# Performance work log

Measured on AMD Instinct MI355X. Metric: run time of the kernel, lower is better.

Reference implementation:

```python
import jax, jax.numpy as jnp
import numpy as np

H = 4
N_PAPER, N_AUTHOR = 100000, 50000
F_IN = 128
HID, OUT = 128, 64  # total channels (per-head = total // H)


def setup_inputs() -> dict:
    key = jax.random.key(0)
    ks = jax.random.split(key, 20)
    inp = {
        'x_paper': jax.random.normal(ks[0], (N_PAPER, F_IN), jnp.float32),
        'x_author': jax.random.normal(ks[1], (N_AUTHOR, F_IN), jnp.float32),
        'src_pp': jax.random.randint(ks[2], (1600000,), 0, N_PAPER, jnp.int32),
        'dst_pp': jax.random.randint(ks[3], (1600000,), 0, N_PAPER, jnp.int32),
        'src_ap': jax.random.randint(ks[4], (800000,), 0, N_AUTHOR, jnp.int32),
        'dst_ap': jax.random.randint(ks[5], (800000,), 0, N_PAPER, jnp.int32),
        'src_pa': jax.random.randint(ks[6], (800000,), 0, N_PAPER, jnp.int32),
        'dst_pa': jax.random.randint(ks[7], (800000,), 0, N_AUTHOR, jnp.int32),
    }
    # Per-edge-type (3 relations) GATConv params, stacked on axis 0.
    s1 = 1.0 / np.sqrt(F_IN)
    s2 = 1.0 / np.sqrt(HID)
    inp['Wsrc1'] = jax.random.normal(ks[8], (3, F_IN, HID), jnp.float32) * s1
    inp['Wdst1'] = jax.random.normal(ks[9], (3, F_IN, HID), jnp.float32) * s1
    inp['asrc1'] = jax.random.normal(ks[10], (3, H, HID // H), jnp.float32) * s1
    inp['adst1'] = jax.random.normal(ks[11], (3, H, HID // H), jnp.float32) * s1
    inp['b1'] = jnp.zeros((3, HID), jnp.float32)
    inp['Wsrc2'] = jax.random.normal(ks[12], (3, HID, OUT), jnp.float32) * s2
    inp['Wdst2'] = jax.random.normal(ks[13], (3, HID, OUT), jnp.float32) * s2
    inp['asrc2'] = jax.random.normal(ks[14], (3, H, OUT // H), jnp.float32) * s2
    inp['adst2'] = jax.random.normal(ks[15], (3, H, OUT // H), jnp.float32) * s2
    inp['b2'] = jnp.zeros((3, OUT), jnp.float32)
    return inp


def gat_conv(xs, xd, src, dst, Ws, Wd, a_s, a_d, b, n_dst):
    """Bipartite GATConv (PyG semantics, add_self_loops=False, concat=True)."""
    C = a_s.shape[-1]
    hs = (xs @ Ws).reshape(xs.shape[0], H, C)   # [Ns,H,C]
    hd = (xd @ Wd).reshape(xd.shape[0], H, C)   # [Nd,H,C]
    es = jnp.sum(hs * a_s, axis=-1)             # [Ns,H]
    ed = jnp.sum(hd * a_d, axis=-1)             # [Nd,H]
    e = jax.nn.leaky_relu(es[src] + ed[dst], negative_slope=0.2)  # [E,H]
    m = jax.ops.segment_max(e, dst, num_segments=n_dst)
    m = jnp.where(jnp.isfinite(m), m, 0.0)
    ee = jnp.exp(e - m[dst])
    denom = jax.ops.segment_sum(ee, dst, num_segments=n_dst)
    alpha = ee / (denom[dst] + 1e-16)           # softmax over incoming edges
    out = jax.ops.segment_sum(alpha[:, :, None] * hs[src], dst, num_segments=n_dst)
    return out.reshape(n_dst, H * C) + b


def reference(x_paper, x_author, src_pp, dst_pp, src_ap, dst_ap, src_pa, dst_pa,
              Wsrc1, Wdst1, asrc1, adst1, b1, Wsrc2, Wdst2, asrc2, adst2, b2):
    def layer(xp, xa, Ws, Wd, a_s, a_d, b):
        # to_hetero: one conv per relation, sum-aggregate per dst node type
        op = gat_conv(xp, xp, src_pp, dst_pp, Ws[0], Wd[0], a_s[0], a_d[0], b[0], N_PAPER)
        op = op + gat_conv(xa, xp, src_ap, dst_ap, Ws[1], Wd[1], a_s[1], a_d[1], b[1], N_PAPER)
        oa = gat_conv(xp, xa, src_pa, dst_pa, Ws[2], Wd[2], a_s[2], a_d[2], b[2], N_AUTHOR)
        return op, oa

    hp, ha = layer(x_paper, x_author, Wsrc1, Wdst1, asrc1, adst1, b1)
    hp, ha = jax.nn.relu(hp), jax.nn.relu(ha)
    op, oa = layer(hp, ha, Wsrc2, Wdst2, asrc2, adst2, b2)
    # concat node types along axis 0: [N_PAPER + N_AUTHOR, OUT]
    return jnp.concatenate([op, oa], axis=0)
```

## Files before the change

### kernel.cpp

```cpp
#include <hip/hip_runtime.h>


#define LEAKY(x) ((x) > 0.f ? (x) : 0.2f * (x))
#define ECH 4096
#define NBMAX 784

typedef _Float16 h8 __attribute__((ext_vector_type(8)));
typedef _Float16 h2 __attribute__((ext_vector_type(2)));
typedef float f4 __attribute__((ext_vector_type(4)));

__launch_bounds__(256)
__global__ void bucket_scatter_chunked(
    const int* __restrict__ s0, const int* __restrict__ d0, int E0,
    int* __restrict__ bc0, int* __restrict__ bt0, int C0, int NB0, int c0,
    const int* __restrict__ s1, const int* __restrict__ d1, int E1,
    int* __restrict__ bc1, int* __restrict__ bt1, int C1, int NB1, int c1,
    const int* __restrict__ s2, const int* __restrict__ d2, int E2,
    int* __restrict__ bc2, int* __restrict__ bt2, int C2, int NB2) {
    __shared__ int lcnt[NBMAX], lbase[NBMAX];
    int ch = blockIdx.x;
    const int* src; const int* dst; int* bc; int* bt; int cap, NB, E;
    if (ch < c0)            { src = s0; dst = d0; bc = bc0; bt = bt0; cap = C0; NB = NB0; E = E0; }
    else if (ch < c0 + c1)  { ch -= c0; src = s1; dst = d1; bc = bc1; bt = bt1; cap = C1; NB = NB1; E = E1; }
    else                    { ch -= c0 + c1; src = s2; dst = d2; bc = bc2; bt = bt2; cap = C2; NB = NB2; E = E2; }
    int t = threadIdx.x;
    int ebeg = ch * ECH;
    int eend = ebeg + ECH < E ? ebeg + ECH : E;

    for (int b = t; b < NB; b += 256) lcnt[b] = 0;
    __syncthreads();
    for (int i = ebeg + t; i < eend; i += 256) atomicAdd(&lcnt[dst[i] >> 7], 1);
    __syncthreads();
    for (int b = t; b < NB; b += 256) {
        int c = lcnt[b];
        lbase[b] = c ? atomicAdd(&bc[b], c) : 0;
        lcnt[b] = 0;
    }
    __syncthreads();
    for (int i = ebeg + t; i < eend; i += 256) {
        int d = dst[i], b = d >> 7;
        int p = lbase[b] + atomicAdd(&lcnt[b], 1);
        if (p < cap) bt[(size_t)b * cap + p] = src[i] | ((d & 127) << 20);
    }
}

__launch_bounds__(256)
__global__ void bucket_build(
    const int* __restrict__ bt0, const int* __restrict__ bc0, int* __restrict__ ss0,
    int* __restrict__ beg0, int* __restrict__ end0, int NB0, int C0, int Nd0,
    const int* __restrict__ bt1, const int* __restrict__ bc1, int* __restrict__ ss1,
    int* __restrict__ beg1, int* __restrict__ end1, int NB1, int C1, int Nd1,
    const int* __restrict__ bt2, const int* __restrict__ bc2, int* __restrict__ ss2,
    int* __restrict__ beg2, int* __restrict__ end2, int NB2, int C2, int Nd2) {
    __shared__ int hist[128], pre[129], cur[128];
    int bb = blockIdx.x;
    const int* bt; const int* bcp; int* ssp; int* bg; int* en; int cap, nd;
    if (bb < NB0)            { bt = bt0; bcp = bc0; ssp = ss0; bg = beg0; en = end0; cap = C0; nd = Nd0; }
    else if (bb < NB0 + NB1) { bb -= NB0; bt = bt1; bcp = bc1; ssp = ss1; bg = beg1; en = end1; cap = C1; nd = Nd1; }
    else                     { bb -= NB0 + NB1; bt = bt2; bcp = bc2; ssp = ss2; bg = beg2; en = end2; cap = C2; nd = Nd2; }
    int tid = threadIdx.x;
    int n = bcp[bb]; if (n > cap) n = cap;
    const int* btb = bt + (size_t)bb * cap;
    int ssbase = bb * cap;
    int dbase = bb << 7;

    if (tid < 128) hist[tid] = 0;
    __syncthreads();
    for (int i = tid; i < n; i += 256) atomicAdd(&hist[btb[i] >> 20], 1);
    __syncthreads();
    if (tid < 128) pre[tid + 1] = hist[tid];
    if (tid == 0) pre[0] = 0;
    __syncthreads();
    for (int off = 1; off < 128; off <<= 1) {
        int v = 0;
        if (tid < 128) {
            int i = tid + 1;
            v = pre[i] + ((i > off) ? pre[i - off] : 0);
        }
        __syncthreads();
        if (tid < 128) pre[tid + 1] = v;
        __syncthreads();
    }
    if (tid < 128) {
        int d = dbase + tid;
        if (d < nd) {
            int b_ = ssbase + pre[tid];
            bg[d] = b_;
            en[d] = b_ + hist[tid];
        }
        cur[tid] = 0;
    }
    __syncthreads();
    for (int i = tid; i < n; i += 256) {
        int v = btb[i];
        int dl = v >> 20;
        int p = atomicAdd(&cur[dl], 1);
        ssp[ssbase + pre[dl] + p] = v & 0xFFFFF;
    }
}

__launch_bounds__(512)
__global__ void prep(const float* __restrict__ Wdst1, const float* __restrict__ adst1,
                     const float* __restrict__ Wdst2, const float* __restrict__ adst2,
                     const float* __restrict__ Wsrc1, const float* __restrict__ Wsrc2,
                     const float* __restrict__ b1, const float* __restrict__ b2,
                     float* __restrict__ WDA, _Float16* __restrict__ Wt,
                     float* __restrict__ bsum) {
    int r = blockIdx.x, t = threadIdx.x;
    if (r < 6) {
        int f = t >> 2, h = t & 3;
        const float* Wd; const float* ad; int Ncol, C;
        if (r < 3) { Wd = Wdst1 + r * 16384; ad = adst1 + r * 128; Ncol = 128; C = 32; }
        else       { Wd = Wdst2 + (r - 3) * 8192; ad = adst2 + (r - 3) * 64; Ncol = 64; C = 16; }
        float s = 0.f;
        for (int c = 0; c < C; ++c) s += Wd[f * Ncol + h * C + c] * ad[h * C + c];
        WDA[r * 512 + f * 4 + h] = s;
    } else if (r < 12) {
        int rr = r - 6;
        const float* W; _Float16* o; int BN;
        if (rr < 3) { W = Wsrc1 + rr * 16384; o = Wt + rr * 16384; BN = 128; }
        else        { W = Wsrc2 + (rr - 3) * 8192; o = Wt + 3 * 16384 + (rr - 3) * 8192; BN = 64; }
        for (int idx = t; idx < BN * 128; idx += 512) {
            int n = idx >> 7, k = idx & 127;
            o[idx] = (_Float16)W[k * BN + n];
        }
    } else {
        if (t < 128) bsum[t] = b1[t] + b1[128 + t];
        else if (t < 192) bsum[128 + (t - 128)] = b2[t - 128] + b2[64 + (t - 128)];
    }
}

__launch_bounds__(256)
__global__ void conv_ed(const float* __restrict__ xp, const float* __restrict__ xa,
                        int NP, int NA, _Float16* __restrict__ xph, _Float16* __restrict__ xah,
                        const float* __restrict__ WDA,
                        float* __restrict__ EDpp, float* __restrict__ EDap,
                        float* __restrict__ EDpa) {
    int wid = blockIdx.x * 4 + (threadIdx.x >> 6);
    if (wid >= NP + NA) return;
    int lane = threadIdx.x & 63;
    const float* x; _Float16* xh; const float4* W0; const float4* W1;
    float* e0p; float* e1p; int row;
    if (wid < NP) { row = wid; x = xp; xh = xph; W0 = (const float4*)WDA;
                    W1 = (const float4*)(WDA + 512); e0p = EDpp; e1p = EDap; }
    else { row = wid - NP; x = xa; xh = xah; W0 = (const float4*)(WDA + 1024);
           W1 = nullptr; e0p = EDpa; e1p = nullptr; }
    float2 xv = *(const float2*)(x + (size_t)row * 128 + lane * 2);
    h2 hv = {(_Float16)xv.x, (_Float16)xv.y};
    *(h2*)(xh + (size_t)row * 128 + lane * 2) = hv;
    float4 a0 = W0[lane * 2], a1 = W0[lane * 2 + 1];
    float4 p = make_float4(xv.x * a0.x + xv.y * a1.x, xv.x * a0.y + xv.y * a1.y,
                           xv.x * a0.z + xv.y * a1.z, xv.x * a0.w + xv.y * a1.w);
    float4 q = make_float4(0.f, 0.f, 0.f, 0.f);
    if (W1) {
        float4 b0 = W1[lane * 2], b1 = W1[lane * 2 + 1];
        q = make_float4(xv.x * b0.x + xv.y * b1.x, xv.x * b0.y + xv.y * b1.y,
                        xv.x * b0.z + xv.y * b1.z, xv.x * b0.w + xv.y * b1.w);
    }
#pragma unroll
    for (int off = 32; off; off >>= 1) {
        p.x += __shfl_xor(p.x, off); p.y += __shfl_xor(p.y, off);
        p.z += __shfl_xor(p.z, off); p.w += __shfl_xor(p.w, off);
        q.x += __shfl_xor(q.x, off); q.y += __shfl_xor(q.y, off);
        q.z += __shfl_xor(q.z, off); q.w += __shfl_xor(q.w, off);
    }
    if (lane == 0) {
        *(float4*)(e0p + (size_t)row * 4) = p;
        if (e1p) *(float4*)(e1p + (size_t)row * 4) = q;
    }
}

template <int BN>
__launch_bounds__(256)
__global__ void gemm3(const _Float16* __restrict__ A0, int M0, const _Float16* __restrict__ W0,
                      const float* __restrict__ as0, _Float16* __restrict__ O0, float* __restrict__ es0,
                      const _Float16* __restrict__ A1, int M1, const _Float16* __restrict__ W1,
                      const float* __restrict__ as1, _Float16* __restrict__ O1, float* __restrict__ es1,
                      const _Float16* __restrict__ A2, int M2, const _Float16* __restrict__ W2,
                      const float* __restrict__ as2, _Float16* __restrict__ O2, float* __restrict__ es2,
                      int t0, int t1) {
    constexpr int NT = BN / 16;
    constexpr int LDA = 136;
    __shared__ _Float16 As[64 * LDA];
    __shared__ _Float16 Ws[BN * LDA];
    int b = blockIdx.x;
    const _Float16* A; const _Float16* Wt; const float* a_s; _Float16* Chs; float* es;
    int M, tile;
    if (b < t0)      { A = A0; M = M0; Wt = W0; a_s = as0; Chs = O0; es = es0; tile = b; }
    else if (b < t1) { A = A1; M = M1; Wt = W1; a_s = as1; Chs = O1; es = es1; tile = b - t0; }
    else             { A = A2; M = M2; Wt = W2; a_s = as2; Chs = O2; es = es2; tile = b - t1; }
    const int tid = threadIdx.x;
    const int wave = tid >> 6, lane = tid & 63;
    const int l15 = lane & 15, quad = lane >> 4;
    const int row0 = tile * 64;
    const int maxr = M - row0;

#pragma unroll
    for (int c = 0; c < 4; ++c) {
        int idx = c * 256 + tid;
        int row = idx >> 4, off = (idx & 15) * 8;
        h8 v = {};
        if (row < maxr) v = *(const h8*)(A + (size_t)(row0 + row) * 128 + off);
        *(h8*)(As + row * LDA + off) = v;
    }
#pragma unroll
    for (int c = 0; c < NT; ++c) {
        int idx = c * 256 + tid;
        int row = idx >> 4, off = (idx & 15) * 8;
        *(h8*)(Ws + row * LDA + off) = *(const h8*)(Wt + (size_t)row * 128 + off);
    }
    __syncthreads();

    f4 acc[NT];
#pragma unroll
    for (int nt = 0; nt < NT; ++nt) acc[nt] = {0.f, 0.f, 0.f, 0.f};

    const _Float16* ap = As + (wave * 16 + l15) * LDA + quad * 8;
#pragma unroll
    for (int k0 = 0; k0 < 128; k0 += 32) {
        h8 a = *(const h8*)(ap + k0);
#pragma unroll
        for (int nt = 0; nt < NT; ++nt) {
            h8 bb = *(const h8*)(Ws + (nt * 16 + l15) * LDA + k0 + quad * 8);
            acc[nt] = __builtin_amdgcn_mfma_f32_16x16x32_f16(a, bb, acc[nt], 0, 0, 0);
        }
    }

    float av[NT];
#pragma unroll
    for (int nt = 0; nt < NT; ++nt) av[nt] = a_s[nt * 16 + l15];
    constexpr int TPH = NT / 4;
#pragma unroll
    for (int r = 0; r < 4; ++r) {
        int row = wave * 16 + quad * 4 + r;
        bool ok = row < maxr;
        if (ok) {
            _Float16* outp = Chs + (size_t)(row0 + row) * BN + l15;
#pragma unroll
            for (int nt = 0; nt < NT; ++nt) outp[nt * 16] = (_Float16)acc[nt][r];
        }
        float p0 = 0.f, p1 = 0.f, p2 = 0.f, p3 = 0.f;
#pragma unroll
        for (int i = 0; i < TPH; ++i) {
            p0 += acc[0 * TPH + i][r] * av[0 * TPH + i];
            p1 += acc[1 * TPH + i][r] * av[1 * TPH + i];
            p2 += acc[2 * TPH + i][r] * av[2 * TPH + i];
            p3 += acc[3 * TPH + i][r] * av[3 * TPH + i];
        }
#pragma unroll
        for (int off = 1; off < 16; off <<= 1) {
            p0 += __shfl_xor(p0, off);
            p1 += __shfl_xor(p1, off);
            p2 += __shfl_xor(p2, off);
            p3 += __shfl_xor(p3, off);
        }
        if (ok && l15 < 4) {
            float pv = (l15 == 0) ? p0 : (l15 == 1) ? p1 : (l15 == 2) ? p2 : p3;
            es[(size_t)(row0 + row) * 4 + l15] = pv;
        }
    }
}

template <int CH>
__device__ __forceinline__ void gat_gather(
    int b0, int e0, const int* __restrict__ ss, const _Float16* __restrict__ hs,
    const float* __restrict__ es, float edh, int lane, int h, int el,
    float& racc0, float& racc1, float& rden) {
    float m = -3e38f, acc0 = 0.f, acc1 = 0.f, den = 0.f;
    for (int base = b0; base < e0; base += 16) {
        int n = e0 - base;
        if (n > 16) n = 16;
        int s = 0;
        float e = -3e38f;
        if (el < n) {
            s = ss[base + el];
            e = es[(size_t)s * 4 + h] + edh;
            e = LEAKY(e);
        }
        float cm = e;
        cm = fmaxf(cm, __shfl_xor(cm, 1));
        cm = fmaxf(cm, __shfl_xor(cm, 2));
        cm = fmaxf(cm, __shfl_xor(cm, 4));
        cm = fmaxf(cm, __shfl_xor(cm, 8));
        float nm = fmaxf(m, cm);
        float f = __expf(m - nm);
        acc0 *= f; acc1 *= f; den *= f;
        m = nm;
        float w = (el < n) ? __expf(e - m) : 0.f;

        int j = 0;
        for (; j + 4 <= n; j += 4) {
            int sa = __shfl(s, j), sb = __shfl(s, j + 1), sc = __shfl(s, j + 2), sd = __shfl(s, j + 3);
            float w0 = __shfl(w, (h << 4) | j);
            float w1 = __shfl(w, (h << 4) | (j + 1));
            float w2 = __shfl(w, (h << 4) | (j + 2));
            float w3 = __shfl(w, (h << 4) | (j + 3));
            if constexpr (CH == 128) {
                h2 v0 = *(const h2*)(hs + (size_t)sa * 128 + lane * 2);
                h2 v1 = *(const h2*)(hs + (size_t)sb * 128 + lane * 2);
                h2 v2 = *(const h2*)(hs + (size_t)sc * 128 + lane * 2);
                h2 v3 = *(const h2*)(hs + (size_t)sd * 128 + lane * 2);
                acc0 += w0 * (float)v0[0] + w1 * (float)v1[0] + w2 * (float)v2[0] + w3 * (float)v3[0];
                acc1 += w0 * (float)v0[1] + w1 * (float)v1[1] + w2 * (float)v2[1] + w3 * (float)v3[1];
            } else {
                acc0 += w0 * (float)hs[(size_t)sa * 64 + lane] + w1 * (float)hs[(size_t)sb * 64 + lane] +
                        w2 * (float)hs[(size_t)sc * 64 + lane] + w3 * (float)hs[(size_t)sd * 64 + lane];
            }
            den += w0 + w1 + w2 + w3;
        }
        for (; j < n; ++j) {
            int sj = __shfl(s, j);
            float wj = __shfl(w, (h << 4) | j);
            if constexpr (CH == 128) {
                h2 v = *(const h2*)(hs + (size_t)sj * 128 + lane * 2);
                acc0 += wj * (float)v[0];
                acc1 += wj * (float)v[1];
            } else {
                acc0 += wj * (float)hs[(size_t)sj * 64 + lane];
            }
            den += wj;
        }
    }
    racc0 = acc0; racc1 = acc1; rden = den;
}

__device__ __forceinline__ void ed_reduce_write(float o0, float o1, const float* wda,
                                                float* edO, int wid, int lane) {
    const float4* W = (const float4*)wda;
    float4 w0 = W[lane * 2], w1 = W[lane * 2 + 1];
    float4 p = make_float4(o0 * w0.x + o1 * w1.x, o0 * w0.y + o1 * w1.y,
                           o0 * w0.z + o1 * w1.z, o0 * w0.w + o1 * w1.w);
#pragma unroll
    for (int off = 32; off; off >>= 1) {
        p.x += __shfl_xor(p.x, off); p.y += __shfl_xor(p.y, off);
        p.z += __shfl_xor(p.z, off); p.w += __shfl_xor(p.w, off);
    }
    if (lane == 0) *(float4*)(edO + (size_t)wid * 4) = p;
}

template <int CH, typename OT>
__launch_bounds__(256)
__global__ void aggregate1(const int* __restrict__ beg, const int* __restrict__ end_,
                           const int* __restrict__ ss, const _Float16* __restrict__ hs,
                           const float* __restrict__ es, const float* __restrict__ ed,
                           const float* __restrict__ bias, OT* __restrict__ out,
                           int Ndst, int relu, const float* __restrict__ wdaO,
                           float* __restrict__ edO) {
    int wid = blockIdx.x * 4 + (threadIdx.x >> 6);
    if (wid >= Ndst) return;
    int lane = threadIdx.x & 63, h = lane >> 4, el = lane & 15;
    float edh = ed[(size_t)wid * 4 + h];
    float a0, a1, dn;
    gat_gather<CH>(beg[wid], end_[wid], ss, hs, es, edh, lane, h, el, a0, a1, dn);
    float inv = 1.f / (dn + 1e-16f);
    if constexpr (CH == 128) {
        float o0 = a0 * inv + bias[lane * 2];
        float o1 = a1 * inv + bias[lane * 2 + 1];
        if (relu) { o0 = fmaxf(o0, 0.f); o1 = fmaxf(o1, 0.f); }
        size_t i0 = (size_t)wid * 128 + lane * 2;
        if constexpr (sizeof(OT) == 2) {
            h2 ov = {(_Float16)o0, (_Float16)o1};
            *(h2*)((_Float16*)out + i0) = ov;
            o0 = (float)ov[0]; o1 = (float)ov[1];
        } else {
            *(float2*)((float*)out + i0) = make_float2(o0, o1);
        }
        if (edO) ed_reduce_write(o0, o1, wdaO, edO, wid, lane);
    } else {
        float o = a0 * inv + bias[lane];
        if (relu) o = fmaxf(o, 0.f);
        out[(size_t)wid * 64 + lane] = (OT)o;
    }
}

template <int CH, typename OT>
__launch_bounds__(256)
__global__ void aggregate2(const int* __restrict__ begA, const int* __restrict__ endA,
                           const int* __restrict__ ssA, const _Float16* __restrict__ hsA,
                           const float* __restrict__ esA, const float* __restrict__ edA,
                           const int* __restrict__ begB, const int* __restrict__ endB,
                           const int* __restrict__ ssB, const _Float16* __restrict__ hsB,
                           const float* __restrict__ esB, const float* __restrict__ edB,
                           const float* __restrict__ bsum, OT* __restrict__ out,
                           int Ndst, int relu,
                           const float* __restrict__ wda1, float* __restrict__ ed1O,
                           const float* __restrict__ wda2, float* __restrict__ ed2O) {
    int wid = blockIdx.x * 4 + (threadIdx.x >> 6);
    if (wid >= Ndst) return;
    int lane = threadIdx.x & 63, h = lane >> 4, el = lane & 15;
    float edhA = edA[(size_t)wid * 4 + h];
    float edhB = edB[(size_t)wid * 4 + h];
    float aA0, aA1, dnA, aB0, aB1, dnB;
    gat_gather<CH>(begA[wid], endA[wid], ssA, hsA, esA, edhA, lane, h, el, aA0, aA1, dnA);
    gat_gather<CH>(begB[wid], endB[wid], ssB, hsB, esB, edhB, lane, h, el, aB0, aB1, dnB);
    float invA = 1.f / (dnA + 1e-16f), invB = 1.f / (dnB + 1e-16f);
    if constexpr (CH == 128) {
        float o0 = aA0 * invA + aB0 * invB + bsum[lane * 2];
        float o1 = aA1 * invA + aB1 * invB + bsum[lane * 2 + 1];
        if (relu) { o0 = fmaxf(o0, 0.f); o1 = fmaxf(o1, 0.f); }
        size_t i0 = (size_t)wid * 128 + lane * 2;
        if constexpr (sizeof(OT) == 2) {
            h2 ov = {(_Float16)o0, (_Float16)o1};
            *(h2*)((_Float16*)out + i0) = ov;
            o0 = (float)ov[0]; o1 = (float)ov[1];
        } else {
            *(float2*)((float*)out + i0) = make_float2(o0, o1);
        }
        if (ed1O) ed_reduce_write(o0, o1, wda1, ed1O, wid, lane);
        if (ed2O) ed_reduce_write(o0, o1, wda2, ed2O, wid, lane);
    } else {
        float o = aA0 * invA + aB0 * invB + bsum[lane];
        if (relu) o = fmaxf(o, 0.f);
        out[(size_t)wid * 64 + lane] = (OT)o;
    }
}

extern "C" void kernel_launch(void* const* d_in, const int* in_sizes, int n_in,
                              void* d_out, int out_size, void* d_ws, size_t ws_size,
                              hipStream_t stream) {
    const float* xp     = (const float*)d_in[0];
    const float* xa     = (const float*)d_in[1];
    const int* src_pp   = (const int*)d_in[2];
    const int* dst_pp   = (const int*)d_in[3];
    const int* src_ap   = (const int*)d_in[4];
    const int* dst_ap   = (const int*)d_in[5];
    const int* src_pa   = (const int*)d_in[6];
    const int* dst_pa   = (const int*)d_in[7];
    const float* Wsrc1  = (const float*)d_in[8];
    const float* Wdst1  = (const float*)d_in[9];
    const float* asrc1  = (const float*)d_in[10];
    const float* adst1  = (const float*)d_in[11];
    const float* b1     = (const float*)d_in[12];
    const float* Wsrc2  = (const float*)d_in[13];
    const float* Wdst2  = (const float*)d_in[14];
    const float* asrc2  = (const float*)d_in[15];
    const float* adst2  = (const float*)d_in[16];
    const float* b2     = (const float*)d_in[17];

    const int NP  = in_sizes[0] / 128;
    const int NA  = in_sizes[1] / 128;
    const int Epp = in_sizes[2];
    const int Eap = in_sizes[4];
    const int Epa = in_sizes[6];

    const int NB0 = (NP + 127) >> 7, NB1 = (NP + 127) >> 7, NB2 = (NA + 127) >> 7;
    auto cap_of = [](int E, int NB) { int m = E / NB; return ((m * 5 / 4 + 128) + 63) & ~63; };
    const int C0 = cap_of(Epp, NB0), C1 = cap_of(Eap, NB1), C2 = cap_of(Epa, NB2);
    const int c0 = (Epp + ECH - 1) / ECH, c1 = (Eap + ECH - 1) / ECH, c2 = (Epa + ECH - 1) / ECH;

    char* w = (char*)d_ws;
    auto alloc = [&](size_t bytes) {
        char* p = w;
        w += (bytes + 255) & ~(size_t)255;
        return p;
    };
    _Float16* xph = (_Float16*)alloc((size_t)NP * 128 * 2);
    _Float16* xah = (_Float16*)alloc((size_t)NA * 128 * 2);
    _Float16* P1h = (_Float16*)alloc((size_t)NP * 128 * 2);
    _Float16* A1h = (_Float16*)alloc((size_t)NA * 128 * 2);
    _Float16* P2h = (_Float16*)alloc((size_t)NP * 128 * 2);
    _Float16* HPh = (_Float16*)alloc((size_t)NP * 128 * 2);
    _Float16* HAh = (_Float16*)alloc((size_t)NA * 128 * 2);
    _Float16* Wt  = (_Float16*)alloc((size_t)(3 * 16384 + 3 * 8192) * 2);
    int*   ss0  = (int*)alloc((size_t)NB0 * C0 * 4);
    int*   ss1  = (int*)alloc((size_t)NB1 * C1 * 4);
    int*   ss2  = (int*)alloc((size_t)NB2 * C2 * 4);
    int*   beg0 = (int*)alloc((size_t)NP * 4);
    int*   end0 = (int*)alloc((size_t)NP * 4);
    int*   beg1 = (int*)alloc((size_t)NP * 4);
    int*   end1 = (int*)alloc((size_t)NP * 4);
    int*   beg2 = (int*)alloc((size_t)NA * 4);
    int*   end2 = (int*)alloc((size_t)NA * 4);
    float* ESp  = (float*)alloc((size_t)NP * 4 * 4);
    float* ESa  = (float*)alloc((size_t)NA * 4 * 4);
    float* ESp2 = (float*)alloc((size_t)NP * 4 * 4);
    float* EDpp = (float*)alloc((size_t)NP * 4 * 4);
    float* EDap = (float*)alloc((size_t)NP * 4 * 4);
    float* EDpa = (float*)alloc((size_t)NA * 4 * 4);
    float* WDA  = (float*)alloc(6 * 512 * 4);
    float* BSUM = (float*)alloc(192 * 4);
    int*   bcnt = (int*)alloc((size_t)(NB0 + NB1 + NB2) * 4);
    int* bt0 = (int*)P1h;
    int* bt1 = bt0 + (size_t)NB0 * C0;
    int* bt2 = bt1 + (size_t)NB1 * C1;

    hipMemsetAsync(bcnt, 0, (size_t)(NB0 + NB1 + NB2) * 4, stream);
    bucket_scatter_chunked<<<c0 + c1 + c2, 256, 0, stream>>>(
        src_pp, dst_pp, Epp, bcnt, bt0, C0, NB0, c0,
        src_ap, dst_ap, Eap, bcnt + NB0, bt1, C1, NB1, c1,
        src_pa, dst_pa, Epa, bcnt + NB0 + NB1, bt2, C2, NB2);
    bucket_build<<<NB0 + NB1 + NB2, 256, 0, stream>>>(
        bt0, bcnt, ss0, beg0, end0, NB0, C0, NP,
        bt1, bcnt + NB0, ss1, beg1, end1, NB1, C1, NP,
        bt2, bcnt + NB0 + NB1, ss2, beg2, end2, NB2, C2, NA);
    prep<<<13, 512, 0, stream>>>(Wdst1, adst1, Wdst2, adst2, Wsrc1, Wsrc2, b1, b2,
                                 WDA, Wt, BSUM);
    conv_ed<<<(NP + NA + 3) / 4, 256, 0, stream>>>(xp, xa, NP, NA, xph, xah, WDA,
                                                   EDpp, EDap, EDpa);

    float* Opap = (float*)d_out;
    float* Oaut = (float*)d_out + (size_t)NP * 64;
    _Float16* Wt1 = Wt;
    _Float16* Wt2 = Wt + 3 * 16384;
    const int TP = (NP + 63) / 64, TA = (NA + 63) / 64;

    gemm3<128><<<TP + TA + TP, 256, 0, stream>>>(
        xph, NP, Wt1, asrc1, P1h, ESp,
        xah, NA, Wt1 + 16384, asrc1 + 128, A1h, ESa,
        xph, NP, Wt1 + 2 * 16384, asrc1 + 2 * 128, P2h, ESp2,
        TP, TP + TA);
    aggregate2<128, _Float16><<<(NP + 3) / 4, 256, 0, stream>>>(
        beg0, end0, ss0, P1h, ESp, EDpp,
        beg1, end1, ss1, A1h, ESa, EDap,
        BSUM, HPh, NP, 1, WDA + 3 * 512, EDpp, WDA + 4 * 512, EDap);
    aggregate1<128, _Float16><<<(NA + 3) / 4, 256, 0, stream>>>(
        beg2, end2, ss2, P2h, ESp2, EDpa, b1 + 2 * 128, HAh, NA, 1,
        WDA + 5 * 512, EDpa);

    gemm3<64><<<TP + TA + TP, 256, 0, stream>>>(
        HPh, NP, Wt2, asrc2, P1h, ESp,
        HAh, NA, Wt2 + 8192, asrc2 + 64, A1h, ESa,
        HPh, NP, Wt2 + 2 * 8192, asrc2 + 2 * 64, P2h, ESp2,
        TP, TP + TA);
    aggregate2<64, float><<<(NP + 3) / 4, 256, 0, stream>>>(
        beg0, end0, ss0, P1h, ESp, EDpp,
        beg1, end1, ss1, A1h, ESa, EDap,
        BSUM + 128, Opap, NP, 0, nullptr, nullptr, nullptr, nullptr);
    aggregate1<64, float><<<(NA + 3) / 4, 256, 0, stream>>>(
        beg2, end2, ss2, P2h, ESp2, EDpa, b2 + 2 * 64, Oaut, NA, 0,
        nullptr, nullptr);
}
```

Measured before the change: 692.2 us.

## Gather multiple edges per wave with 16-byte vector loads in GAT aggregation

Restructures the per-destination gather so that each lane loads 8 half-precision channels at once (16 bytes), with the wave split into groups that process several edges concurrently (4 for 128-channel, 8 for 64-channel rows). Partial sums are then combined with cross-lane shuffles. The epilogue, bias add and attention-dot reduction are rewritten to work on 8 values per lane. This targets latency and instruction overhead from many small 2- and 4-byte scattered loads. In exchange it adds shuffle reductions, higher register use, and partial idle lanes when a node's edge count is not a multiple of the group count.

```diff
diff --git a/kernel.cpp b/kernel.cpp
--- a/kernel.cpp
+++ b/kernel.cpp
@@ -265,8 +265,18 @@
 __device__ __forceinline__ void gat_gather(
     int b0, int e0, const int* __restrict__ ss, const _Float16* __restrict__ hs,
     const float* __restrict__ es, float edh, int lane, int h, int el,
-    float& racc0, float& racc1, float& rden) {
-    float m = -3e38f, acc0 = 0.f, acc1 = 0.f, den = 0.f;
+    float* __restrict__ acc, float& rden) {
+    constexpr int GL = (CH == 128) ? 16 : 8;
+    constexpr int NG = 64 / GL;
+    const int cl = lane & (GL - 1);
+    const int g = lane >> (CH == 128 ? 4 : 3);
+    const int hh = cl >> (CH == 128 ? 2 : 1);
+    const int wsrc = (hh << 4) | g;
+    const int fsrc = hh << 4;
+    float m = -3e38f, den = 0.f;
+#pragma unroll
+    for (int i = 0; i < 8; ++i) acc[i] = 0.f;
+
     for (int base = b0; base < e0; base += 16) {
         int n = e0 - base;
         if (n > 16) n = 16;
@@ -284,58 +294,86 @@
         cm = fmaxf(cm, __shfl_xor(cm, 8));
         float nm = fmaxf(m, cm);
         float f = __expf(m - nm);
-        acc0 *= f; acc1 *= f; den *= f;
         m = nm;
         float w = (el < n) ? __expf(e - m) : 0.f;
-
-        int j = 0;
-        for (; j + 4 <= n; j += 4) {
-            int sa = __shfl(s, j), sb = __shfl(s, j + 1), sc = __shfl(s, j + 2), sd = __shfl(s, j + 3);
-            float w0 = __shfl(w, (h << 4) | j);
-            float w1 = __shfl(w, (h << 4) | (j + 1));
-            float w2 = __shfl(w, (h << 4) | (j + 2));
-            float w3 = __shfl(w, (h << 4) | (j + 3));
-            if constexpr (CH == 128) {
-                h2 v0 = *(const h2*)(hs + (size_t)sa * 128 + lane * 2);
-                h2 v1 = *(const h2*)(hs + (size_t)sb * 128 + lane * 2);
-                h2 v2 = *(const h2*)(hs + (size_t)sc * 128 + lane * 2);
-                h2 v3 = *(const h2*)(hs + (size_t)sd * 128 + lane * 2);
-                acc0 += w0 * (float)v0[0] + w1 * (float)v1[0] + w2 * (float)v2[0] + w3 * (float)v3[0];
-                acc1 += w0 * (float)v0[1] + w1 * (float)v1[1] + w2 * (float)v2[1] + w3 * (float)v3[1];
-            } else {
-                acc0 += w0 * (float)hs[(size_t)sa * 64 + lane] + w1 * (float)hs[(size_t)sb * 64 + lane] +
-                        w2 * (float)hs[(size_t)sc * 64 + lane] + w3 * (float)hs[(size_t)sd * 64 + lane];
-            }
-            den += w0 + w1 + w2 + w3;
-        }
-        for (; j < n; ++j) {
-            int sj = __shfl(s, j);
-            float wj = __shfl(w, (h << 4) | j);
-            if constexpr (CH == 128) {
-                h2 v = *(const h2*)(hs + (size_t)sj * 128 + lane * 2);
-                acc0 += wj * (float)v[0];
-                acc1 += wj * (float)v[1];
-            } else {
-                acc0 += wj * (float)hs[(size_t)sj * 64 + lane];
-            }
+        float fg = __shfl(f, fsrc);
+#pragma unroll
+        for (int i = 0; i < 8; ++i) acc[i] *= fg;
+        den *= fg;
+
+        for (int j = 0; j < n; j += NG) {
+            int sj = __shfl(s, j + g);
+            float wj = __shfl(w, wsrc + j);
+            const h8 v = *(const h8*)(hs + (size_t)sj * CH + cl * 8);
+#pragma unroll
+            for (int i = 0; i < 8; ++i) acc[i] = fmaf(wj, (float)v[i], acc[i]);
             den += wj;
         }
     }
-    racc0 = acc0; racc1 = acc1; rden = den;
-}
-
-__device__ __forceinline__ void ed_reduce_write(float o0, float o1, const float* wda,
-                                                float* edO, int wid, int lane) {
+    if (CH == 64) {
+#pragma unroll
+        for (int i = 0; i < 8; ++i) acc[i] += __shfl_xor(acc[i], 8);
+        den += __shfl_xor(den, 8);
+    }
+#pragma unroll
+    for (int i = 0; i < 8; ++i) acc[i] += __shfl_xor(acc[i], 16);
+    den += __shfl_xor(den, 16);
+#pragma unroll
+    for (int i = 0; i < 8; ++i) acc[i] += __shfl_xor(acc[i], 32);
+    den += __shfl_xor(den, 32);
+    rden = den;
+}
+
+__device__ __forceinline__ void ed_reduce_write(const float* __restrict__ o,
+                                                const float* __restrict__ wda,
+                                                float* __restrict__ edO,
+                                                int wid, int cl, int lane) {
     const float4* W = (const float4*)wda;
-    float4 w0 = W[lane * 2], w1 = W[lane * 2 + 1];
-    float4 p = make_float4(o0 * w0.x + o1 * w1.x, o0 * w0.y + o1 * w1.y,
-                           o0 * w0.z + o1 * w1.z, o0 * w0.w + o1 * w1.w);
-#pragma unroll
-    for (int off = 32; off; off >>= 1) {
-        p.x += __shfl_xor(p.x, off); p.y += __shfl_xor(p.y, off);
-        p.z += __shfl_xor(p.z, off); p.w += __shfl_xor(p.w, off);
+    float4 p = make_float4(0.f, 0.f, 0.f, 0.f);
+#pragma unroll
+    for (int i = 0; i < 8; ++i) {
+        float4 wv = W[cl * 8 + i];
+        p.x = fmaf(o[i], wv.x, p.x);
+        p.y = fmaf(o[i], wv.y, p.y);
+        p.z = fmaf(o[i], wv.z, p.z);
+        p.w = fmaf(o[i], wv.w, p.w);
+    }
+#pragma unroll
+    for (int off = 1; off < 16; off <<= 1) {
+        p.x += __shfl_xor(p.x, off);
+        p.y += __shfl_xor(p.y, off);
+        p.z += __shfl_xor(p.z, off);
+        p.w += __shfl_xor(p.w, off);
     }
     if (lane == 0) *(float4*)(edO + (size_t)wid * 4) = p;
+}
+
+template <int CH, typename OT>
+__device__ __forceinline__ void epilogue_write(float* __restrict__ o, int lane, int cl,
+                                               int relu, OT* __restrict__ out, int wid,
+                                               const float* __restrict__ wda1, float* __restrict__ ed1O,
+                                               const float* __restrict__ wda2, float* __restrict__ ed2O) {
+    constexpr int GL = (CH == 128) ? 16 : 8;
+    if (relu) {
+#pragma unroll
+        for (int i = 0; i < 8; ++i) o[i] = fmaxf(o[i], 0.f);
+    }
+    if constexpr (sizeof(OT) == 2) {
+        h8 ov;
+#pragma unroll
+        for (int i = 0; i < 8; ++i) ov[i] = (_Float16)o[i];
+        if (lane < GL) *(h8*)((_Float16*)out + (size_t)wid * CH + cl * 8) = ov;
+#pragma unroll
+        for (int i = 0; i < 8; ++i) o[i] = (float)ov[i];
+    } else {
+        if (lane < GL) {
+            float* op = (float*)out + (size_t)wid * CH + cl * 8;
+            *(float4*)op = make_float4(o[0], o[1], o[2], o[3]);
+            *(float4*)(op + 4) = make_float4(o[4], o[5], o[6], o[7]);
+        }
+    }
+    if (ed1O) ed_reduce_write(o, wda1, ed1O, wid, cl, lane);
+    if (ed2O) ed_reduce_write(o, wda2, ed2O, wid, cl, lane);
 }
 
 template <int CH, typename OT>
@@ -349,28 +387,20 @@
     int wid = blockIdx.x * 4 + (threadIdx.x >> 6);
     if (wid >= Ndst) return;
     int lane = threadIdx.x & 63, h = lane >> 4, el = lane & 15;
+    constexpr int GL = (CH == 128) ? 16 : 8;
+    int cl = lane & (GL - 1);
     float edh = ed[(size_t)wid * 4 + h];
-    float a0, a1, dn;
-    gat_gather<CH>(beg[wid], end_[wid], ss, hs, es, edh, lane, h, el, a0, a1, dn);
+    float a[8], dn;
+    gat_gather<CH>(beg[wid], end_[wid], ss, hs, es, edh, lane, h, el, a, dn);
     float inv = 1.f / (dn + 1e-16f);
-    if constexpr (CH == 128) {
-        float o0 = a0 * inv + bias[lane * 2];
-        float o1 = a1 * inv + bias[lane * 2 + 1];
-        if (relu) { o0 = fmaxf(o0, 0.f); o1 = fmaxf(o1, 0.f); }
-        size_t i0 = (size_t)wid * 128 + lane * 2;
-        if constexpr (sizeof(OT) == 2) {
-            h2 ov = {(_Float16)o0, (_Float16)o1};
-            *(h2*)((_Float16*)out + i0) = ov;
-            o0 = (float)ov[0]; o1 = (float)ov[1];
-        } else {
-            *(float2*)((float*)out + i0) = make_float2(o0, o1);
-        }
-        if (edO) ed_reduce_write(o0, o1, wdaO, edO, wid, lane);
-    } else {
-        float o = a0 * inv + bias[lane];
-        if (relu) o = fmaxf(o, 0.f);
-        out[(size_t)wid * 64 + lane] = (OT)o;
-    }
+    const float4* bv = (const float4*)bias + cl * 2;
+    float4 b0 = bv[0], b1 = bv[1];
+    float o[8];
+    o[0] = fmaf(a[0], inv, b0.x); o[1] = fmaf(a[1], inv, b0.y);
+    o[2] = fmaf(a[2], inv, b0.z); o[3] = fmaf(a[3], inv, b0.w);
+    o[4] = fmaf(a[4], inv, b1.x); o[5] = fmaf(a[5], inv, b1.y);
+    o[6] = fmaf(a[6], inv, b1.z); o[7] = fmaf(a[7], inv, b1.w);
+    epilogue_write<CH, OT>(o, lane, cl, relu, out, wid, wdaO, edO, nullptr, nullptr);
 }
 
 template <int CH, typename OT>
@@ -388,31 +418,26 @@
     int wid = blockIdx.x * 4 + (threadIdx.x >> 6);
     if (wid >= Ndst) return;
     int lane = threadIdx.x & 63, h = lane >> 4, el = lane & 15;
+    constexpr int GL = (CH == 128) ? 16 : 8;
+    int cl = lane & (GL - 1);
     float edhA = edA[(size_t)wid * 4 + h];
     float edhB = edB[(size_t)wid * 4 + h];
-    float aA0, aA1, dnA, aB0, aB1, dnB;
-    gat_gather<CH>(begA[wid], endA[wid], ssA, hsA, esA, edhA, lane, h, el, aA0, aA1, dnA);
-    gat_gather<CH>(begB[wid], endB[wid], ssB, hsB, esB, edhB, lane, h, el, aB0, aB1, dnB);
+    float aA[8], aB[8], dnA, dnB;
+    gat_gather<CH>(begA[wid], endA[wid], ssA, hsA, esA, edhA, lane, h, el, aA, dnA);
+    gat_gather<CH>(begB[wid], endB[wid], ssB, hsB, esB, edhB, lane, h, el, aB, dnB);
     float invA = 1.f / (dnA + 1e-16f), invB = 1.f / (dnB + 1e-16f);
-    if constexpr (CH == 128) {
-        float o0 = aA0 * invA + aB0 * invB + bsum[lane * 2];
-        float o1 = aA1 * invA + aB1 * invB + bsum[lane * 2 + 1];
-        if (relu) { o0 = fmaxf(o0, 0.f); o1 = fmaxf(o1, 0.f); }
-        size_t i0 = (size_t)wid * 128 + lane * 2;
-        if constexpr (sizeof(OT) == 2) {
-            h2 ov = {(_Float16)o0, (_Float16)o1};
-            *(h2*)((_Float16*)out + i0) = ov;
-            o0 = (float)ov[0]; o1 = (float)ov[1];
-        } else {
-            *(float2*)((float*)out + i0) = make_float2(o0, o1);
-        }
-        if (ed1O) ed_reduce_write(o0, o1, wda1, ed1O, wid, lane);
-        if (ed2O) ed_reduce_write(o0, o1, wda2, ed2O, wid, lane);
-    } else {
-        float o = aA0 * invA + aB0 * invB + bsum[lane];
-        if (relu) o = fmaxf(o, 0.f);
-        out[(size_t)wid * 64 + lane] = (OT)o;
-    }
+    const float4* bv = (const float4*)bsum + cl * 2;
+    float4 b0 = bv[0], b1 = bv[1];
+    float o[8];
+    o[0] = fmaf(aA[0], invA, fmaf(aB[0], invB, b0.x));
+    o[1] = fmaf(aA[1], invA, fmaf(aB[1], invB, b0.y));
+    o[2] = fmaf(aA[2], invA, fmaf(aB[2], invB, b0.z));
+    o[3] = fmaf(aA[3], invA, fmaf(aB[3], invB, b0.w));
+    o[4] = fmaf(aA[4], invA, fmaf(aB[4], invB, b1.x));
+    o[5] = fmaf(aA[5], invA, fmaf(aB[5], invB, b1.y));
+    o[6] = fmaf(aA[6], invA, fmaf(aB[6], invB, b1.z));
+    o[7] = fmaf(aA[7], invA, fmaf(aB[7], invB, b1.w));
+    epilogue_write<CH, OT>(o, lane, cl, relu, out, wid, wda1, ed1O, wda2, ed2O);
 }
 
 extern "C" void kernel_launch(void* const* d_in, const int* in_sizes, int n_in,
```

Measured after the change: 799.4 us. 15.5% more time.
